# Kernel tuning notes

Measured on AMD Instinct MI355X. Metric: run time of the kernel, lower is better.

Reference implementation:

```python
import jax, jax.numpy as jnp
import numpy as np

B, T, C = 32, 2048, 1024  # batch, seq_len (<= block_size), n_embd
HEAD_SIZE = 128


def setup_inputs() -> dict:
    key = jax.random.key(0)
    kx, kk, kq, kv = jax.random.split(key, 4)
    std = 0.02  # CustomLinear init: normal(0, 0.02)
    return {
        "x": jax.random.normal(kx, (B, T, C), dtype=jnp.float32),
        "Wk": jax.random.normal(kk, (HEAD_SIZE, C), dtype=jnp.float32) * std,
        "Wq": jax.random.normal(kq, (HEAD_SIZE, C), dtype=jnp.float32) * std,
        "Wv": jax.random.normal(kv, (HEAD_SIZE, C), dtype=jnp.float32) * std,
    }


def reference(x, Wk, Wq, Wv):
    # x: [B, T, C]; W*: [head_size, C] (torch Linear layout, no bias)
    Bb, Tt, Cc = x.shape
    k = jnp.einsum("btc,hc->bth", x, Wk)
    q = jnp.einsum("btc,hc->bth", x, Wq)
    v = jnp.einsum("btc,hc->bth", x, Wv)
    # NOTE: original scales by C**-0.5 (n_embd), not head_size**-0.5
    wei = jnp.einsum("bth,bsh->bts", q, k) * (Cc ** -0.5)
    causal = jnp.tril(jnp.ones((Tt, Tt), dtype=bool))  # tril[:T,:T]
    wei = jnp.where(causal, wei, -jnp.inf)
    wei = jax.nn.softmax(wei, axis=-1)
    return jnp.einsum("bts,bsh->bth", wei, v)  # [B, T, head_size]
```

## Files before the change

### kernel.cpp

```cpp
#include <hip/hip_runtime.h>
#include <hip/hip_bf16.h>

typedef __bf16 bf8_t __attribute__((ext_vector_type(8)));
typedef __bf16 bf4_t __attribute__((ext_vector_type(4)));
typedef float f4_t __attribute__((ext_vector_type(4)));

#define B_ 32
#define T_ 2048
#define C_ 1024
#define H_ 128

__global__ __launch_bounds__(256) void wconv_kernel(
    const float* __restrict__ Wk, const float* __restrict__ Wq, const float* __restrict__ Wv,
    __bf16* __restrict__ Wr)
{
    const int e  = (blockIdx.x * 256 + threadIdx.x) * 8;
    const int kk = e & 31;
    const int lr = (e >> 5) & 15;
    const int ks = (e >> 9) & 31;
    const int cg = e >> 14;
    const int col = cg * 16 + lr;
    const int k   = ks * 32 + kk;
    const float* W = (col < 128) ? Wk : (col < 256) ? Wq : Wv;
    const float* p = W + (size_t)(col & 127) * C_ + k;
    float4 f0 = *(const float4*)p;
    float4 f1 = *(const float4*)(p + 4);
    bf8_t o;
    o[0] = (__bf16)f0.x; o[1] = (__bf16)f0.y; o[2] = (__bf16)f0.z; o[3] = (__bf16)f0.w;
    o[4] = (__bf16)f1.x; o[5] = (__bf16)f1.y; o[6] = (__bf16)f1.z; o[7] = (__bf16)f1.w;
    *(bf8_t*)(Wr + e) = o;
}

__global__ __launch_bounds__(256) void proj_kernel(
    const float* __restrict__ x, const __bf16* __restrict__ Wr,
    __bf16* __restrict__ Kb, __bf16* __restrict__ Qb, __bf16* __restrict__ VtG)
{
    __shared__ __bf16 As[128 * 64];
    __shared__ __bf16 Bs[2][16 * 512];

    const int bid  = blockIdx.x;
    const int xcd  = bid & 7;
    const int slot = bid >> 3;
    const int nt   = slot % 3;
    const int m0   = ((slot / 3) * 8 + xcd) * 128;
    const int tid  = threadIdx.x;
    const int lane = tid & 63;
    const int w    = tid >> 6;
    const int wqm  = w >> 1;
    const int wqn  = w & 1;
    const int lr   = lane & 15;
    const int quad = lane >> 4;

    f4_t acc[4][4];
    #pragma unroll
    for (int mi = 0; mi < 4; mi++)
        #pragma unroll
        for (int ni = 0; ni < 4; ni++) acc[mi][ni] = f4_t{0.f, 0.f, 0.f, 0.f};

    float4 pf[8];

#define LOADA(t) { _Pragma("unroll") \
    for (int i_ = 0; i_ < 8; ++i_) { \
        const int u_ = i_ * 256 + tid; \
        pf[i_] = *(const float4*)(x + (size_t)(m0 + (u_ >> 4)) * C_ + (t) * 64 + (u_ & 15) * 4); } }

#define WRITEA { _Pragma("unroll") \
    for (int i_ = 0; i_ < 8; ++i_) { \
        const int u_ = i_ * 256 + tid; \
        const int r_ = u_ >> 4; \
        float4 f_ = pf[i_]; \
        *(bf4_t*)&As[r_ * 64 + ((((u_ & 15) * 4)) ^ ((r_ & 7) * 8))] = \
            bf4_t{(__bf16)f_.x, (__bf16)f_.y, (__bf16)f_.z, (__bf16)f_.w}; } }

#define STAGEB(t, bsel) { _Pragma("unroll") \
    for (int i_ = 0; i_ < 4; ++i_) { \
        const int ci_ = i_ * 4 + w; \
        const __bf16* src_ = Wr + ((size_t)((nt * 8 + (ci_ >> 1)) * 32 + (t) * 2 + (ci_ & 1)) << 9) + lane * 8; \
        __builtin_amdgcn_global_load_lds( \
            (const __attribute__((address_space(1))) void*)src_, \
            (__attribute__((address_space(3))) void*)&Bs[bsel][ci_ << 9], 16, 0, 0); } }

    LOADA(0)
    STAGEB(0, 0)
    WRITEA
    __syncthreads();

    #pragma unroll 2
    for (int t = 0; t < 16; ++t) {
        const int bsel = t & 1;
        if (t < 15) {
            LOADA(t + 1)
            STAGEB(t + 1, bsel ^ 1)
        }
        #pragma unroll
        for (int kh = 0; kh < 2; ++kh) {
            bf8_t af[4], bfr[4];
            #pragma unroll
            for (int mi = 0; mi < 4; ++mi) {
                const int row = wqm * 64 + mi * 16 + lr;
                af[mi] = *(const bf8_t*)&As[row * 64 + ((kh * 32 + quad * 8) ^ ((row & 7) * 8))];
            }
            #pragma unroll
            for (int ni = 0; ni < 4; ++ni) {
                const int ch = (wqn * 4 + ni) * 2 + kh;
                bfr[ni] = *(const bf8_t*)&Bs[bsel][ch * 512 + lr * 32 + quad * 8];
            }
            if (nt < 2) {
                #pragma unroll
                for (int mi = 0; mi < 4; ++mi)
                    #pragma unroll
                    for (int ni = 0; ni < 4; ++ni)
                        acc[mi][ni] = __builtin_amdgcn_mfma_f32_16x16x32_bf16(af[mi], bfr[ni], acc[mi][ni], 0, 0, 0);
            } else {
                #pragma unroll
                for (int mi = 0; mi < 4; ++mi)
                    #pragma unroll
                    for (int ni = 0; ni < 4; ++ni)
                        acc[mi][ni] = __builtin_amdgcn_mfma_f32_16x16x32_bf16(bfr[ni], af[mi], acc[mi][ni], 0, 0, 0);
            }
        }
        __syncthreads();
        if (t < 15) {
            WRITEA
            __syncthreads();
        }
    }

#undef LOADA
#undef WRITEA
#undef STAGEB

    if (nt < 2) {
        __bf16* Out = nt ? Qb : Kb;
        #pragma unroll
        for (int ni = 0; ni < 4; ++ni)
            #pragma unroll
            for (int mi = 0; mi < 4; ++mi) {
                const int col = wqn * 64 + ni * 16 + lr;
                #pragma unroll
                for (int r = 0; r < 4; ++r) {
                    const int row = m0 + wqm * 64 + mi * 16 + quad * 4 + r;
                    Out[(size_t)row * H_ + col] = (__bf16)acc[mi][ni][r];
                }
            }
    } else {
        const int bb = m0 >> 11;
        const int t0 = m0 & (T_ - 1);
        #pragma unroll
        for (int ni = 0; ni < 4; ++ni)
            #pragma unroll
            for (int mi = 0; mi < 4; ++mi) {
                const int tok = t0 + wqm * 64 + mi * 16 + lr;
                #pragma unroll
                for (int r = 0; r < 4; ++r) {
                    const int h = wqn * 64 + ni * 16 + quad * 4 + r;
                    VtG[(size_t)bb * H_ * T_ + (size_t)h * T_ + tok] = (__bf16)acc[mi][ni][r];
                }
            }
    }
}

__global__ __launch_bounds__(256, 2) void flash_kernel(
    const __bf16* __restrict__ Qb, const __bf16* __restrict__ Kb,
    const __bf16* __restrict__ VtG, float* __restrict__ Out)
{
    __shared__ __bf16 Ks[64][136];
    __shared__ __bf16 Vt[128][72];
    __shared__ __bf16 Ps[64][72];

    const int b  = blockIdx.x;
    const int qp = blockIdx.y;
    const size_t kqbase = (size_t)b * T_ * H_;
    const size_t vbase  = (size_t)b * H_ * T_;

    const int tid  = threadIdx.x;
    const int lane = tid & 63;
    const int w    = tid >> 6;
    const int lr   = lane & 15;
    const int quad = lane >> 4;

    const float sc = 0.03125f * 1.4426950408889634f;

    int kR[4], kC[4], vH[4], vS[4];
    #pragma unroll
    for (int i = 0; i < 4; i++) {
        const int u = tid + i * 256;
        kR[i] = u >> 4;  kC[i] = (u & 15) << 3;
        vH[i] = u >> 3;  vS[i] = (u & 7) << 3;
    }

    bf8_t kr[4], vr[4];
    #pragma unroll
    for (int i = 0; i < 4; i++) {
        kr[i] = *(const bf8_t*)(Kb + kqbase + (size_t)kR[i] * H_ + kC[i]);
        vr[i] = *(const bf8_t*)(VtG + vbase + (size_t)vH[i] * T_ + vS[i]);
    }

    for (int seg = 0; seg < 2; ++seg) {
        const int qt   = seg ? (31 - qp) : qp;
        const int jmax = qt;

        bf8_t qf[4];
        {
            const __bf16* qpr = Qb + kqbase + (size_t)(qt * 64 + w * 16 + lr) * H_ + quad * 8;
            #pragma unroll
            for (int ks = 0; ks < 4; ks++) qf[ks] = *(const bf8_t*)(qpr + ks * 32);
        }

        f4_t o[8];
        #pragma unroll
        for (int n = 0; n < 8; n++) o[n] = f4_t{0.f, 0.f, 0.f, 0.f};
        float ls = 0.f;

        for (int j = 0; j <= jmax; ++j) {
            __syncthreads();
            #pragma unroll
            for (int i = 0; i < 4; i++) {
                *(bf8_t*)&Ks[kR[i]][kC[i]] = kr[i];
                *(bf8_t*)&Vt[vH[i]][vS[i]] = vr[i];
            }
            __syncthreads();
            {
                const int s0 = (j < jmax) ? (j + 1) * 64 : 0;
                #pragma unroll
                for (int i = 0; i < 4; i++) {
                    kr[i] = *(const bf8_t*)(Kb + kqbase + (size_t)(s0 + kR[i]) * H_ + kC[i]);
                    vr[i] = *(const bf8_t*)(VtG + vbase + (size_t)vH[i] * T_ + s0 + vS[i]);
                }
            }

            f4_t s4[4];
            #pragma unroll
            for (int n = 0; n < 4; n++) s4[n] = f4_t{0.f, 0.f, 0.f, 0.f};
            #pragma unroll
            for (int ks = 0; ks < 4; ks++)
                #pragma unroll
                for (int n = 0; n < 4; n++) {
                    bf8_t kf = *(const bf8_t*)&Ks[n * 16 + lr][ks * 32 + quad * 8];
                    s4[n] = __builtin_amdgcn_mfma_f32_16x16x32_bf16(kf, qf[ks], s4[n], 0, 0, 0);
                }

            const bool dm = (j == jmax);
            const int qg = w * 16 + lr;
            #pragma unroll
            for (int n = 0; n < 4; n++) {
                bf4_t pk;
                #pragma unroll
                for (int r = 0; r < 4; r++) {
                    float p = __builtin_exp2f(s4[n][r] * sc);
                    if (dm && (n * 16 + quad * 4 + r) > qg) p = 0.f;
                    ls += p;
                    pk[r] = (__bf16)p;
                }
                *(bf4_t*)&Ps[w * 16 + lr][n * 16 + quad * 4] = pk;
            }

            #pragma unroll
            for (int ks = 0; ks < 2; ks++) {
                bf8_t pfr = *(const bf8_t*)&Ps[w * 16 + lr][ks * 32 + quad * 8];
                #pragma unroll
                for (int n = 0; n < 8; n++) {
                    bf8_t vf = *(const bf8_t*)&Vt[n * 16 + lr][ks * 32 + quad * 8];
                    o[n] = __builtin_amdgcn_mfma_f32_16x16x32_bf16(pfr, vf, o[n], 0, 0, 0);
                }
            }
        }

        float v = ls;
        v += __shfl_xor(v, 16);
        v += __shfl_xor(v, 32);
        const float iv = 1.f / v;
        float inv[4];
        #pragma unroll
        for (int r = 0; r < 4; r++) inv[r] = __shfl(iv, quad * 4 + r);

        #pragma unroll
        for (int n = 0; n < 8; n++) {
            const int col = n * 16 + lr;
            #pragma unroll
            for (int r = 0; r < 4; r++) {
                const int row = qt * 64 + w * 16 + quad * 4 + r;
                Out[kqbase + (size_t)row * H_ + col] = o[n][r] * inv[r];
            }
        }
    }
}

extern "C" void kernel_launch(void* const* d_in, const int* in_sizes, int n_in,
                              void* d_out, int out_size, void* d_ws, size_t ws_size,
                              hipStream_t stream) {
    const float* x  = (const float*)d_in[0];
    const float* Wk = (const float*)d_in[1];
    const float* Wq = (const float*)d_in[2];
    const float* Wv = (const float*)d_in[3];
    float* out = (float*)d_out;

    const size_t n_kqv = (size_t)B_ * T_ * H_;
    __bf16* Kb  = (__bf16*)d_ws;
    __bf16* Qb  = Kb + n_kqv;
    __bf16* VtG = Qb + n_kqv;
    __bf16* Wr  = VtG + n_kqv;

    wconv_kernel<<<dim3(192), 256, 0, stream>>>(Wk, Wq, Wv, Wr);
    proj_kernel<<<dim3(512 * 3), 256, 0, stream>>>(x, Wr, Kb, Qb, VtG);
    flash_kernel<<<dim3(32, 16), 256, 0, stream>>>(Qb, Kb, VtG, out);
}
```

Baseline: 470.5 us.

## Store K/Q/V in MFMA fragment layout and read flash operands directly from global

The projection kernel now writes K, Q and V into a pre-tiled fragment layout, so each lane's MFMA operand is one contiguous 16-byte load. The flash kernel drops the K and V shared-memory staging and its barriers, reads fragments straight from global memory (relying on L2 reuse), and raises the occupancy hint to 4 blocks per CU. It also launches one block per (batch, query tile), 1024 blocks in a heaviest-first interleaved order, instead of pairing tiles to balance causal work. The trade-off is losing the register prefetch of the next tile and exposing global-load latency directly in the MFMA loop.

```diff
diff --git a/kernel.cpp b/kernel.cpp
--- a/kernel.cpp
+++ b/kernel.cpp
@@ -33,7 +33,7 @@
 
 __global__ __launch_bounds__(256) void proj_kernel(
     const float* __restrict__ x, const __bf16* __restrict__ Wr,
-    __bf16* __restrict__ Kb, __bf16* __restrict__ Qb, __bf16* __restrict__ VtG)
+    __bf16* __restrict__ KF, __bf16* __restrict__ QF, __bf16* __restrict__ VF)
 {
     __shared__ __bf16 As[128 * 64];
     __shared__ __bf16 Bs[2][16 * 512];
@@ -131,18 +131,22 @@
 #undef STAGEB
 
     if (nt < 2) {
-        __bf16* Out = nt ? Qb : Kb;
-        #pragma unroll
-        for (int ni = 0; ni < 4; ++ni)
-            #pragma unroll
-            for (int mi = 0; mi < 4; ++mi) {
-                const int col = wqn * 64 + ni * 16 + lr;
+        __bf16* OutF = nt ? QF : KF;
+        #pragma unroll
+        for (int ni = 0; ni < 4; ++ni) {
+            const int col = wqn * 64 + ni * 16 + lr;
+            const int ks  = col >> 5;
+            const int kk  = col & 31;
+            #pragma unroll
+            for (int mi = 0; mi < 4; ++mi)
                 #pragma unroll
                 for (int r = 0; r < 4; ++r) {
                     const int row = m0 + wqm * 64 + mi * 16 + quad * 4 + r;
-                    Out[(size_t)row * H_ + col] = (__bf16)acc[mi][ni][r];
+                    const int bb2 = row >> 11, t2 = row & 2047;
+                    OutF[((((size_t)bb2 * 32 + (t2 >> 6)) * 4 + ((t2 >> 4) & 3)) * 4 + ks) * 512
+                         + (t2 & 15) * 32 + kk] = (__bf16)acc[mi][ni][r];
                 }
-            }
+        }
     } else {
         const int bb = m0 >> 11;
         const int t0 = m0 & (T_ - 1);
@@ -154,134 +158,103 @@
                 #pragma unroll
                 for (int r = 0; r < 4; ++r) {
                     const int h = wqn * 64 + ni * 16 + quad * 4 + r;
-                    VtG[(size_t)bb * H_ * T_ + (size_t)h * T_ + tok] = (__bf16)acc[mi][ni][r];
+                    VF[((((size_t)bb * 32 + (tok >> 6)) * 8 + (h >> 4)) * 2 + ((tok & 63) >> 5)) * 512
+                       + (h & 15) * 32 + (tok & 31)] = (__bf16)acc[mi][ni][r];
                 }
             }
     }
 }
 
-__global__ __launch_bounds__(256, 2) void flash_kernel(
-    const __bf16* __restrict__ Qb, const __bf16* __restrict__ Kb,
-    const __bf16* __restrict__ VtG, float* __restrict__ Out)
+__global__ __launch_bounds__(256, 4) void flash_kernel(
+    const __bf16* __restrict__ QF, const __bf16* __restrict__ KF,
+    const __bf16* __restrict__ VF, float* __restrict__ Out)
 {
-    __shared__ __bf16 Ks[64][136];
-    __shared__ __bf16 Vt[128][72];
     __shared__ __bf16 Ps[64][72];
 
-    const int b  = blockIdx.x;
-    const int qp = blockIdx.y;
-    const size_t kqbase = (size_t)b * T_ * H_;
-    const size_t vbase  = (size_t)b * H_ * T_;
+    const int bid = blockIdx.x;
+    const int b   = bid & 31;
+    const int s   = bid >> 5;
+    const int qt  = (s < 8) ? (31 - s) : (s < 16) ? (s + 8) : (s < 24) ? (31 - s) : (s - 24);
 
     const int tid  = threadIdx.x;
     const int lane = tid & 63;
     const int w    = tid >> 6;
     const int lr   = lane & 15;
     const int quad = lane >> 4;
+    const int fo   = lr * 32 + quad * 8;
 
     const float sc = 0.03125f * 1.4426950408889634f;
-
-    int kR[4], kC[4], vH[4], vS[4];
-    #pragma unroll
-    for (int i = 0; i < 4; i++) {
-        const int u = tid + i * 256;
-        kR[i] = u >> 4;  kC[i] = (u & 15) << 3;
-        vH[i] = u >> 3;  vS[i] = (u & 7) << 3;
-    }
-
-    bf8_t kr[4], vr[4];
-    #pragma unroll
-    for (int i = 0; i < 4; i++) {
-        kr[i] = *(const bf8_t*)(Kb + kqbase + (size_t)kR[i] * H_ + kC[i]);
-        vr[i] = *(const bf8_t*)(VtG + vbase + (size_t)vH[i] * T_ + vS[i]);
-    }
-
-    for (int seg = 0; seg < 2; ++seg) {
-        const int qt   = seg ? (31 - qp) : qp;
-        const int jmax = qt;
-
-        bf8_t qf[4];
-        {
-            const __bf16* qpr = Qb + kqbase + (size_t)(qt * 64 + w * 16 + lr) * H_ + quad * 8;
-            #pragma unroll
-            for (int ks = 0; ks < 4; ks++) qf[ks] = *(const bf8_t*)(qpr + ks * 32);
-        }
-
-        f4_t o[8];
-        #pragma unroll
-        for (int n = 0; n < 8; n++) o[n] = f4_t{0.f, 0.f, 0.f, 0.f};
-        float ls = 0.f;
-
-        for (int j = 0; j <= jmax; ++j) {
-            __syncthreads();
-            #pragma unroll
-            for (int i = 0; i < 4; i++) {
-                *(bf8_t*)&Ks[kR[i]][kC[i]] = kr[i];
-                *(bf8_t*)&Vt[vH[i]][vS[i]] = vr[i];
-            }
-            __syncthreads();
-            {
-                const int s0 = (j < jmax) ? (j + 1) * 64 : 0;
-                #pragma unroll
-                for (int i = 0; i < 4; i++) {
-                    kr[i] = *(const bf8_t*)(Kb + kqbase + (size_t)(s0 + kR[i]) * H_ + kC[i]);
-                    vr[i] = *(const bf8_t*)(VtG + vbase + (size_t)vH[i] * T_ + s0 + vS[i]);
-                }
-            }
-
-            f4_t s4[4];
-            #pragma unroll
-            for (int n = 0; n < 4; n++) s4[n] = f4_t{0.f, 0.f, 0.f, 0.f};
-            #pragma unroll
-            for (int ks = 0; ks < 4; ks++)
-                #pragma unroll
-                for (int n = 0; n < 4; n++) {
-                    bf8_t kf = *(const bf8_t*)&Ks[n * 16 + lr][ks * 32 + quad * 8];
-                    s4[n] = __builtin_amdgcn_mfma_f32_16x16x32_bf16(kf, qf[ks], s4[n], 0, 0, 0);
-                }
-
-            const bool dm = (j == jmax);
-            const int qg = w * 16 + lr;
+    const int jmax = qt;
+
+    bf8_t qf[4];
+    {
+        const __bf16* qp = QF + (((size_t)(b * 32 + qt) * 4 + w) * 4) * 512 + fo;
+        #pragma unroll
+        for (int ks = 0; ks < 4; ks++) qf[ks] = *(const bf8_t*)(qp + ks * 512);
+    }
+
+    f4_t o[8];
+    #pragma unroll
+    for (int n = 0; n < 8; n++) o[n] = f4_t{0.f, 0.f, 0.f, 0.f};
+    float ls = 0.f;
+
+    for (int j = 0; j <= jmax; ++j) {
+        const __bf16* kb = KF + ((size_t)(b * 32 + j) * 16) * 512 + fo;
+        const __bf16* vb = VF + ((size_t)(b * 32 + j) * 16) * 512 + fo;
+
+        f4_t s4[4];
+        #pragma unroll
+        for (int n = 0; n < 4; n++) s4[n] = f4_t{0.f, 0.f, 0.f, 0.f};
+        #pragma unroll
+        for (int ks = 0; ks < 4; ks++)
             #pragma unroll
             for (int n = 0; n < 4; n++) {
-                bf4_t pk;
-                #pragma unroll
-                for (int r = 0; r < 4; r++) {
-                    float p = __builtin_exp2f(s4[n][r] * sc);
-                    if (dm && (n * 16 + quad * 4 + r) > qg) p = 0.f;
-                    ls += p;
-                    pk[r] = (__bf16)p;
-                }
-                *(bf4_t*)&Ps[w * 16 + lr][n * 16 + quad * 4] = pk;
-            }
-
-            #pragma unroll
-            for (int ks = 0; ks < 2; ks++) {
-                bf8_t pfr = *(const bf8_t*)&Ps[w * 16 + lr][ks * 32 + quad * 8];
-                #pragma unroll
-                for (int n = 0; n < 8; n++) {
-                    bf8_t vf = *(const bf8_t*)&Vt[n * 16 + lr][ks * 32 + quad * 8];
-                    o[n] = __builtin_amdgcn_mfma_f32_16x16x32_bf16(pfr, vf, o[n], 0, 0, 0);
-                }
-            }
-        }
-
-        float v = ls;
-        v += __shfl_xor(v, 16);
-        v += __shfl_xor(v, 32);
-        const float iv = 1.f / v;
-        float inv[4];
-        #pragma unroll
-        for (int r = 0; r < 4; r++) inv[r] = __shfl(iv, quad * 4 + r);
-
-        #pragma unroll
-        for (int n = 0; n < 8; n++) {
-            const int col = n * 16 + lr;
+                bf8_t kf = *(const bf8_t*)(kb + (n * 4 + ks) * 512);
+                s4[n] = __builtin_amdgcn_mfma_f32_16x16x32_bf16(kf, qf[ks], s4[n], 0, 0, 0);
+            }
+
+        const bool dm = (j == jmax);
+        const int qg = w * 16 + lr;
+        #pragma unroll
+        for (int n = 0; n < 4; n++) {
+            bf4_t pk;
             #pragma unroll
             for (int r = 0; r < 4; r++) {
-                const int row = qt * 64 + w * 16 + quad * 4 + r;
-                Out[kqbase + (size_t)row * H_ + col] = o[n][r] * inv[r];
-            }
+                float p = __builtin_exp2f(s4[n][r] * sc);
+                if (dm && (n * 16 + quad * 4 + r) > qg) p = 0.f;
+                ls += p;
+                pk[r] = (__bf16)p;
+            }
+            *(bf4_t*)&Ps[w * 16 + lr][n * 16 + quad * 4] = pk;
+        }
+
+        #pragma unroll
+        for (int ks = 0; ks < 2; ks++) {
+            bf8_t pfr = *(const bf8_t*)&Ps[w * 16 + lr][ks * 32 + quad * 8];
+            #pragma unroll
+            for (int n = 0; n < 8; n++) {
+                bf8_t vf = *(const bf8_t*)(vb + (n * 2 + ks) * 512);
+                o[n] = __builtin_amdgcn_mfma_f32_16x16x32_bf16(pfr, vf, o[n], 0, 0, 0);
+            }
+        }
+    }
+
+    float v = ls;
+    v += __shfl_xor(v, 16);
+    v += __shfl_xor(v, 32);
+    const float iv = 1.f / v;
+    float inv[4];
+    #pragma unroll
+    for (int r = 0; r < 4; r++) inv[r] = __shfl(iv, quad * 4 + r);
+
+    const size_t obase = (size_t)b * T_ * H_;
+    #pragma unroll
+    for (int n = 0; n < 8; n++) {
+        const int col = n * 16 + lr;
+        #pragma unroll
+        for (int r = 0; r < 4; r++) {
+            const int row = qt * 64 + w * 16 + quad * 4 + r;
+            Out[obase + (size_t)row * H_ + col] = o[n][r] * inv[r];
         }
     }
 }
@@ -296,12 +269,12 @@
     float* out = (float*)d_out;
 
     const size_t n_kqv = (size_t)B_ * T_ * H_;
-    __bf16* Kb  = (__bf16*)d_ws;
-    __bf16* Qb  = Kb + n_kqv;
-    __bf16* VtG = Qb + n_kqv;
-    __bf16* Wr  = VtG + n_kqv;
+    __bf16* KF = (__bf16*)d_ws;
+    __bf16* QF = KF + n_kqv;
+    __bf16* VF = QF + n_kqv;
+    __bf16* Wr = VF + n_kqv;
 
     wconv_kernel<<<dim3(192), 256, 0, stream>>>(Wk, Wq, Wv, Wr);
-    proj_kernel<<<dim3(512 * 3), 256, 0, stream>>>(x, Wr, Kb, Qb, VtG);
-    flash_kernel<<<dim3(32, 16), 256, 0, stream>>>(Qb, Kb, VtG, out);
-}
+    proj_kernel<<<dim3(512 * 3), 256, 0, stream>>>(x, Wr, KF, QF, VF);
+    flash_kernel<<<dim3(1024), 256, 0, stream>>>(QF, KF, VF, out);
+}
```

New measurement: 569.3 us. 1.21x slower.
